# Kernel optimization log

Measured on AMD Instinct MI355X. Metric: run time of the kernel, lower is better.

The kernel has to match this reference:

```python
import jax, jax.numpy as jnp
import numpy as np

BATCH, C_IN, C_OUT, N_GRID, N_MODES = 64, 64, 64, 8192, 64
SCALE = 1.0 / (C_IN * C_OUT)


def setup_inputs() -> dict:
    key = jax.random.key(0)
    k1, k2, k3 = jax.random.split(key, 3)
    lhss = jax.random.normal(k1, (BATCH, C_IN, N_GRID), dtype=jnp.float32)
    # torch.rand on cfloat draws real and imag uniformly in [0,1), then scaled
    w_real = SCALE * jax.random.uniform(k2, (C_IN, C_OUT, N_MODES), dtype=jnp.float32)
    w_imag = SCALE * jax.random.uniform(k3, (C_IN, C_OUT, N_MODES), dtype=jnp.float32)
    return {"lhss": lhss, "w_real": w_real, "w_imag": w_imag}


def reference(lhss, w_real, w_imag):
    n = lhss.shape[-1]
    n_freq = n // 2 + 1  # rfft output length
    weights = w_real + 1j * w_imag  # (c_in, c_out, modes), complex64
    xf = jnp.fft.rfft(lhss)  # (b, c_in, n_freq) complex
    # complex channel-mixing on the first N_MODES frequency bins only
    mixed = jnp.einsum("bix,iox->box", xf[:, :, :N_MODES], weights)
    # zero-pad remaining high-frequency bins, then inverse rfft
    res = jnp.zeros((lhss.shape[0], weights.shape[1], n_freq), dtype=mixed.dtype)
    res = res.at[:, :, :N_MODES].set(mixed)
    return jnp.fft.irfft(res, n=n)
```

## Files before the change

kernel.cpp:

```cpp
#include <hip/hip_runtime.h>
#include <hip/hip_bf16.h>

#define NG 8192
#define NB 64
#define CI 64
#define CO 64
#define NM 64
#define NFJ 128
#define NROWS 4096

typedef __bf16 bf16x8 __attribute__((ext_vector_type(8)));
typedef float f32x4 __attribute__((ext_vector_type(4)));

#define GLOAD_LDS16(gsrc, ldst)                                                   \
    __builtin_amdgcn_global_load_lds(                                             \
        (const __attribute__((address_space(1))) void*)(gsrc),                    \
        (__attribute__((address_space(3))) void*)(ldst), 16, 0, 0)


__global__ __launch_bounds__(256) void sc_prep(const float* __restrict__ wr,
                                               const float* __restrict__ wi,
                                               __bf16* __restrict__ Ft,
                                               __bf16* __restrict__ Ginv,
                                               __bf16* __restrict__ Wtf) {
    __shared__ __align__(16) __bf16 wlds[16384];
    const float W0 = 6.2831853071795864769f / (float)NG;
    if (blockIdx.x >= 64) {
        int idx = (blockIdx.x - 64) * 256 + threadIdx.x;
        if (idx < 128 * NG) {
            int j = idx >> 13, pos = idx & (NG - 1);
            int blk = pos >> 6, g = (pos >> 3) & 7, e = pos & 7;
            int ksrc = (blk << 6) + (((g ^ (j & 7)) << 3) | e);
            int m = j >> 1;
            int t = (m * ksrc) & (NG - 1);
            float s, c;
            __sincosf((float)t * W0, &s, &c);
            Ft[idx] = (__bf16)((j & 1) ? -s : c);
        } else {
            int i2 = idx - 128 * NG;
            int n = i2 >> 7, pos = i2 & 127;
            int g = pos >> 3, e = pos & 7;
            int psrc = ((g ^ (n & 15)) << 3) | e;
            int m = psrc >> 1, im = psrc & 1;
            int t = (m * n) & (NG - 1);
            float s, c;
            __sincosf((float)t * W0, &s, &c);
            float v;
            if (im) v = (m == 0) ? 0.0f : (-2.0f / NG) * s;
            else    v = ((m == 0) ? 1.0f : 2.0f) / NG * c;
            Ginv[i2] = (__bf16)v;
        }
    } else {
        const int m = blockIdx.x;
        const int t = threadIdx.x;
        const int o = t & 63, q = t >> 6;
        const int ot = o >> 4, l = o & 15;
        float wrv[16], wiv[16];
        #pragma unroll
        for (int cc = 0; cc < 16; ++cc) {
            int ci = q * 16 + cc;
            wrv[cc] = wr[((size_t)ci * 64 + o) * 64 + m];
            wiv[cc] = wi[((size_t)ci * 64 + o) * 64 + m];
        }
        #pragma unroll
        for (int cc = 0; cc < 16; ++cc) {
            int ci = q * 16 + cc;
            int ksa = ci >> 5, ksb = 2 + ksa;
            int kg = (ci >> 3) & 3, e = ci & 7;
            int pos = (kg * 16 + l) * 8 + e;
            wlds[(0*16 + ksa*4 + ot)*512 + pos] = (__bf16)wrv[cc];
            wlds[(0*16 + ksb*4 + ot)*512 + pos] = (__bf16)(-wiv[cc]);
            wlds[(1*16 + ksa*4 + ot)*512 + pos] = (__bf16)wiv[cc];
            wlds[(1*16 + ksb*4 + ot)*512 + pos] = (__bf16)wrv[cc];
        }
        __syncthreads();
        const uint4* src = (const uint4*)wlds;
        uint4* dst = (uint4*)(Wtf + (size_t)m * 16384);
        #pragma unroll
        for (int s = 0; s < 8; ++s)
            dst[s * 256 + t] = src[s * 256 + t];
    }
}

__global__ __launch_bounds__(256) void sc_dft(const float* __restrict__ A,
                                              const __bf16* __restrict__ Ft,
                                              float* __restrict__ XFp,
                                              int nsteps) {
    __shared__ __align__(16) char smem[40960];
    char* A0 = smem;
    char* A1 = smem + 4096;
    char* F0 = smem + 8192;
    char* F1 = smem + 24576;

    const int tid = threadIdx.x;
    const int w = tid >> 6, lane = tid & 63;
    const int l15 = lane & 15, kg = lane >> 4;
    const int wm = w >> 1, wn = w & 1;
    const int rt = blockIdx.x & 127, sp = blockIdx.x >> 7;
    const int r0 = rt * 32;
    const size_t kb0 = (size_t)sp * nsteps * 64;
    const int swz = l15 & 7;

    float4 av[2];
    f32x4 acc[4] = {};

    auto issueA = [&](int step) {
        size_t kb = kb0 + (size_t)step * 64;
        #pragma unroll
        for (int s = 0; s < 2; ++s) {
            int c = s * 256 + tid;
            av[s] = *(const float4*)(A + (size_t)(r0 + (c >> 4)) * NG + kb + (c & 15) * 4);
        }
    };
    auto writeA = [&](char* Ab) {
        #pragma unroll
        for (int s = 0; s < 2; ++s) {
            int c = s * 256 + tid, row = c >> 4, cq = c & 15;
            union { __bf16 h[4]; uint2 u; } cv;
            cv.h[0] = (__bf16)av[s].x; cv.h[1] = (__bf16)av[s].y;
            cv.h[2] = (__bf16)av[s].z; cv.h[3] = (__bf16)av[s].w;
            *(uint2*)(Ab + row * 128 + (((cq >> 1) ^ (row & 7)) << 4) + ((cq & 1) << 3)) = cv.u;
        }
    };
    auto stageF = [&](int step, char* Fb) {
        size_t kb = kb0 + (size_t)step * 64;
        #pragma unroll
        for (int s = 0; s < 4; ++s) {
            int cc = s * 256 + tid;
            GLOAD_LDS16(Ft + (size_t)(cc >> 3) * NG + kb + (cc & 7) * 8, Fb + cc * 16);
        }
    };
    auto compute = [&](const char* Ab, const char* Fb) {
        #pragma unroll
        for (int ks2 = 0; ks2 < 2; ++ks2) {
            bf16x8 a, b[4];
            a = *(const bf16x8*)(Ab + (wm*16 + l15) * 128 +
                                 (((ks2*4 + kg) ^ swz) << 4));
            #pragma unroll
            for (int jt = 0; jt < 4; ++jt)
                b[jt] = *(const bf16x8*)(Fb + (wn*64 + jt*16 + l15) * 128 +
                                         (((ks2*4 + kg) ^ swz) << 4));
            #pragma unroll
            for (int jt = 0; jt < 4; ++jt)
                acc[jt] = __builtin_amdgcn_mfma_f32_16x16x32_bf16(
                    a, b[jt], acc[jt], 0, 0, 0);
        }
    };

    issueA(0); stageF(0, F0); writeA(A0);
    __syncthreads();
    for (int t = 0; t < nsteps; ++t) {
        char* Ac = (t & 1) ? A1 : A0;
        char* Fc = (t & 1) ? F1 : F0;
        char* An = (t & 1) ? A0 : A1;
        char* Fn = (t & 1) ? F0 : F1;
        if (t + 1 < nsteps) { issueA(t + 1); stageF(t + 1, Fn); }
        compute(Ac, Fc);
        if (t + 1 < nsteps) writeA(An);
        __syncthreads();
    }
    #pragma unroll
    for (int jt = 0; jt < 4; ++jt)
        *(f32x4*)(XFp + ((size_t)sp * NFJ + wn*64 + jt*16 + l15) * NROWS +
                  (r0 + wm*16 + kg*4)) = acc[jt];
}

__global__ __launch_bounds__(256) void sc_mix(const float* __restrict__ XFp,
                                              const __bf16* __restrict__ Wtf,
                                              __bf16* __restrict__ M2, int nsplit) {
    __shared__ __align__(16) char at[4096];
    const int t = threadIdx.x;
    const int k = blockIdx.x >> 2, bq = blockIdx.x & 3;
    const int lane = t & 63, ot = t >> 6;
    const int l15 = lane & 15, kg = lane >> 4;

    const int c = t >> 7, t127 = t & 127;
    f32x4 s0 = {}, s1 = {};
    {
        const float* src = XFp + (size_t)(2*k + c) * NROWS + bq*1024 + t127*8;
        const size_t pstride = (size_t)NFJ * NROWS;
        if (nsplit == 8) {
            #pragma unroll
            for (int p = 0; p < 8; ++p) {
                s0 += *(const f32x4*)(src + p*pstride);
                s1 += *(const f32x4*)(src + p*pstride + 4);
            }
        } else {
            for (int p = 0; p < nsplit; ++p) {
                s0 += *(const f32x4*)(src + p*pstride);
                s1 += *(const f32x4*)(src + p*pstride + 4);
            }
        }
    }
    {
        const int bl = t127 >> 3;
        const int i0 = (t127 & 7) * 8;
        union { __bf16 h[8]; uint4 u; } cv;
        cv.h[0]=(__bf16)s0[0]; cv.h[1]=(__bf16)s0[1];
        cv.h[2]=(__bf16)s0[2]; cv.h[3]=(__bf16)s0[3];
        cv.h[4]=(__bf16)s1[0]; cv.h[5]=(__bf16)s1[1];
        cv.h[6]=(__bf16)s1[2]; cv.h[7]=(__bf16)s1[3];
        *(uint4*)(at + bl*256 + ((((c*64 + i0) >> 3) ^ bl) << 4)) = cv.u;
    }
    __syncthreads();

    bf16x8 a[4];
    #pragma unroll
    for (int ks = 0; ks < 4; ++ks)
        a[ks] = *(const bf16x8*)(at + l15*256 + (((ks*4 + kg) ^ l15) << 4));

    f32x4 accR = {}, accI = {};
    #pragma unroll
    for (int ks = 0; ks < 4; ++ks) {
        bf16x8 b0 = *(const bf16x8*)(Wtf + (size_t)(((k*2+0)*4+ks)*4+ot)*512 + lane*8);
        accR = __builtin_amdgcn_mfma_f32_16x16x32_bf16(a[ks], b0, accR, 0, 0, 0);
    }
    #pragma unroll
    for (int ks = 0; ks < 4; ++ks) {
        bf16x8 b1 = *(const bf16x8*)(Wtf + (size_t)(((k*2+1)*4+ks)*4+ot)*512 + lane*8);
        accI = __builtin_amdgcn_mfma_f32_16x16x32_bf16(a[ks], b1, accI, 0, 0, 0);
    }
    #pragma unroll
    for (int rr = 0; rr < 4; ++rr) {
        int bg = bq*16 + kg*4 + rr;
        size_t r = (size_t)bg * CO + ot*16 + l15;
        ushort2 pk;
        pk.x = __builtin_bit_cast(unsigned short, (__bf16)accR[rr]);
        pk.y = __builtin_bit_cast(unsigned short, (__bf16)accI[rr]);
        *(ushort2*)(M2 + r * NFJ + 2 * k) = pk;
    }
}

__global__ __launch_bounds__(512) void sc_idft(const __bf16* __restrict__ M2,
                                               const __bf16* __restrict__ Ginv,
                                               float* __restrict__ out) {
    __shared__ __align__(16) char gls[32768];
    const int tid = threadIdx.x;
    const int w = tid >> 6, lane = tid & 63;
    const int l15 = lane & 15, kg = lane >> 4;
    const int wm = w >> 1;
    const int wn = w & 1;
    const int r0 = (blockIdx.x >> 6) * 128;
    const int n0 = (blockIdx.x & 63) * 128;

    #pragma unroll
    for (int s = 0; s < 4; ++s) {
        int cc = s * 512 + tid;
        GLOAD_LDS16(Ginv + (size_t)n0 * NFJ + cc * 8, gls + cc * 16);
    }

    bf16x8 af[2][4];
    #pragma unroll
    for (int mt = 0; mt < 2; ++mt)
        #pragma unroll
        for (int ks = 0; ks < 4; ++ks)
            af[mt][ks] = *(const bf16x8*)(M2 + (size_t)(r0 + wm*32 + mt*16 + l15) * NFJ +
                                          ks*32 + kg*8);
    __syncthreads();

    f32x4 acc[2][4] = {};
    #pragma unroll
    for (int nt = 0; nt < 4; ++nt) {
        int row = wn*64 + nt*16 + l15;
        bf16x8 bfr[4];
        #pragma unroll
        for (int ks = 0; ks < 4; ++ks)
            bfr[ks] = *(const bf16x8*)(gls + row * 256 + (((ks*4 + kg) ^ (row & 15)) << 4));
        #pragma unroll
        for (int mt = 0; mt < 2; ++mt)
            #pragma unroll
            for (int ks = 0; ks < 4; ++ks)
                acc[mt][nt] = __builtin_amdgcn_mfma_f32_16x16x32_bf16(
                    bfr[ks], af[mt][ks], acc[mt][nt], 0, 0, 0);
    }
    #pragma unroll
    for (int mt = 0; mt < 2; ++mt)
        #pragma unroll
        for (int nt = 0; nt < 4; ++nt)
            *(f32x4*)(out + (size_t)(r0 + wm*32 + mt*16 + l15) * NG +
                      n0 + wn*64 + nt*16 + kg*4) = acc[mt][nt];
}

extern "C" void kernel_launch(void* const* d_in, const int* in_sizes, int n_in,
                              void* d_out, int out_size, void* d_ws, size_t ws_size,
                              hipStream_t stream) {
    const float* lhss = (const float*)d_in[0];
    const float* w_real = (const float*)d_in[1];
    const float* w_imag = (const float*)d_in[2];
    float* out = (float*)d_out;

    char* ws = (char*)d_ws;
    __bf16* Ft_sw   = (__bf16*)ws;
    __bf16* Ginv_sw = (__bf16*)(ws + (2u << 20));
    __bf16* M2      = (__bf16*)(ws + (6u << 20));
    __bf16* Wtf     = (__bf16*)(ws + (7u << 20));
    float*  XFp     = (float*) (ws + (9u << 20));

    int split;
    if      (ws_size >= (25u << 20)) split = 8;
    else if (ws_size >= (17u << 20)) split = 4;
    else if (ws_size >= (13u << 20)) split = 2;
    else                             split = 1;
    int nsteps = 128 / split;

    sc_prep<<<8256, 256, 0, stream>>>(w_real, w_imag, Ft_sw, Ginv_sw, Wtf);
    sc_dft<<<128 * split, 256, 0, stream>>>(lhss, Ft_sw, XFp, nsteps);
    sc_mix<<<256, 256, 0, stream>>>(XFp, Wtf, M2, split);
    sc_idft<<<2048, 512, 0, stream>>>(M2, Ginv_sw, out);
}
```

Before: 105.8 us.

## Double DFT block row tile and stage F through registers instead of LDS-direct loads

```diff
diff --git a/kernel.cpp b/kernel.cpp
--- a/kernel.cpp
+++ b/kernel.cpp
@@ -86,83 +86,100 @@
                                               const __bf16* __restrict__ Ft,
                                               float* __restrict__ XFp,
                                               int nsteps) {
-    __shared__ __align__(16) char smem[40960];
-    char* A0 = smem;
-    char* A1 = smem + 4096;
-    char* F0 = smem + 8192;
-    char* F1 = smem + 24576;
+    __shared__ __align__(16) char smem[49152];
+    char* Ab0 = smem;
+    char* Ab1 = smem + 8192;
+    char* Fb0 = smem + 16384;
+    char* Fb1 = smem + 32768;
 
     const int tid = threadIdx.x;
     const int w = tid >> 6, lane = tid & 63;
     const int l15 = lane & 15, kg = lane >> 4;
     const int wm = w >> 1, wn = w & 1;
-    const int rt = blockIdx.x & 127, sp = blockIdx.x >> 7;
-    const int r0 = rt * 32;
+    const int rt = blockIdx.x & 63, sp = blockIdx.x >> 6;
+    const int r0 = rt * 64;
     const size_t kb0 = (size_t)sp * nsteps * 64;
     const int swz = l15 & 7;
 
-    float4 av[2];
-    f32x4 acc[4] = {};
-
-    auto issueA = [&](int step) {
+    float4 av0[4], av1[4];
+    uint4  fv0[4], fv1[4];
+    f32x4 acc[2][4] = {};
+
+    auto loadA = [&](int step, float4 (&av)[4]) {
         size_t kb = kb0 + (size_t)step * 64;
         #pragma unroll
-        for (int s = 0; s < 2; ++s) {
+        for (int s = 0; s < 4; ++s) {
             int c = s * 256 + tid;
             av[s] = *(const float4*)(A + (size_t)(r0 + (c >> 4)) * NG + kb + (c & 15) * 4);
         }
     };
-    auto writeA = [&](char* Ab) {
-        #pragma unroll
-        for (int s = 0; s < 2; ++s) {
+    auto loadF = [&](int step, uint4 (&fv)[4]) {
+        size_t kb = kb0 + (size_t)step * 64;
+        #pragma unroll
+        for (int s = 0; s < 4; ++s) {
+            int cc = s * 256 + tid;
+            fv[s] = *(const uint4*)(Ft + (size_t)(cc >> 3) * NG + kb + (cc & 7) * 8);
+        }
+    };
+    auto writeT = [&](const float4 (&av)[4], const uint4 (&fv)[4],
+                      char* Ad, char* Fd) {
+        #pragma unroll
+        for (int s = 0; s < 4; ++s) {
             int c = s * 256 + tid, row = c >> 4, cq = c & 15;
             union { __bf16 h[4]; uint2 u; } cv;
             cv.h[0] = (__bf16)av[s].x; cv.h[1] = (__bf16)av[s].y;
             cv.h[2] = (__bf16)av[s].z; cv.h[3] = (__bf16)av[s].w;
-            *(uint2*)(Ab + row * 128 + (((cq >> 1) ^ (row & 7)) << 4) + ((cq & 1) << 3)) = cv.u;
-        }
-    };
-    auto stageF = [&](int step, char* Fb) {
-        size_t kb = kb0 + (size_t)step * 64;
+            *(uint2*)(Ad + row * 128 + (((cq >> 1) ^ (row & 7)) << 4) + ((cq & 1) << 3)) = cv.u;
+        }
         #pragma unroll
         for (int s = 0; s < 4; ++s) {
             int cc = s * 256 + tid;
-            GLOAD_LDS16(Ft + (size_t)(cc >> 3) * NG + kb + (cc & 7) * 8, Fb + cc * 16);
+            *(uint4*)(Fd + cc * 16) = fv[s];
         }
     };
     auto compute = [&](const char* Ab, const char* Fb) {
         #pragma unroll
         for (int ks2 = 0; ks2 < 2; ++ks2) {
-            bf16x8 a, b[4];
-            a = *(const bf16x8*)(Ab + (wm*16 + l15) * 128 +
-                                 (((ks2*4 + kg) ^ swz) << 4));
+            bf16x8 a[2], b[4];
+            #pragma unroll
+            for (int mt = 0; mt < 2; ++mt)
+                a[mt] = *(const bf16x8*)(Ab + (wm*32 + mt*16 + l15) * 128 +
+                                         (((ks2*4 + kg) ^ swz) << 4));
             #pragma unroll
             for (int jt = 0; jt < 4; ++jt)
                 b[jt] = *(const bf16x8*)(Fb + (wn*64 + jt*16 + l15) * 128 +
                                          (((ks2*4 + kg) ^ swz) << 4));
             #pragma unroll
-            for (int jt = 0; jt < 4; ++jt)
-                acc[jt] = __builtin_amdgcn_mfma_f32_16x16x32_bf16(
-                    a, b[jt], acc[jt], 0, 0, 0);
+            for (int mt = 0; mt < 2; ++mt)
+                #pragma unroll
+                for (int jt = 0; jt < 4; ++jt)
+                    acc[mt][jt] = __builtin_amdgcn_mfma_f32_16x16x32_bf16(
+                        a[mt], b[jt], acc[mt][jt], 0, 0, 0);
         }
     };
 
-    issueA(0); stageF(0, F0); writeA(A0);
+    loadA(0, av0); loadF(0, fv0);
+    writeT(av0, fv0, Ab0, Fb0);
+    loadA(1, av1); loadF(1, fv1);
     __syncthreads();
-    for (int t = 0; t < nsteps; ++t) {
-        char* Ac = (t & 1) ? A1 : A0;
-        char* Fc = (t & 1) ? F1 : F0;
-        char* An = (t & 1) ? A0 : A1;
-        char* Fn = (t & 1) ? F0 : F1;
-        if (t + 1 < nsteps) { issueA(t + 1); stageF(t + 1, Fn); }
-        compute(Ac, Fc);
-        if (t + 1 < nsteps) writeA(An);
+
+    for (int t = 0; t < nsteps; t += 2) {
+        if (t + 2 < nsteps) { loadA(t + 2, av0); loadF(t + 2, fv0); }
+        compute(Ab0, Fb0);
+        writeT(av1, fv1, Ab1, Fb1);
         __syncthreads();
-    }
-    #pragma unroll
-    for (int jt = 0; jt < 4; ++jt)
-        *(f32x4*)(XFp + ((size_t)sp * NFJ + wn*64 + jt*16 + l15) * NROWS +
-                  (r0 + wm*16 + kg*4)) = acc[jt];
+        if (t + 3 < nsteps) { loadA(t + 3, av1); loadF(t + 3, fv1); }
+        compute(Ab1, Fb1);
+        if (t + 2 < nsteps) writeT(av0, fv0, Ab0, Fb0);
+        __syncthreads();
+    }
+
+    #pragma unroll
+    for (int mt = 0; mt < 2; ++mt)
+        #pragma unroll
+        for (int jt = 0; jt < 4; ++jt)
+            *(f32x4*)(XFp + ((size_t)sp * NFJ + wn*64 + jt*16 + l15) * NROWS +
+                      (r0 + wm*32 + mt*16 + kg*4)) = acc[mt][jt];
 }
 
 __global__ __launch_bounds__(256) void sc_mix(const float* __restrict__ XFp,
@@ -304,7 +321,7 @@
     int nsteps = 128 / split;
 
     sc_prep<<<8256, 256, 0, stream>>>(w_real, w_imag, Ft_sw, Ginv_sw, Wtf);
-    sc_dft<<<128 * split, 256, 0, stream>>>(lhss, Ft_sw, XFp, nsteps);
+    sc_dft<<<64 * split, 256, 0, stream>>>(lhss, Ft_sw, XFp, nsteps);
     sc_mix<<<256, 256, 0, stream>>>(XFp, Wtf, M2, split);
     sc_idft<<<2048, 512, 0, stream>>>(M2, Ginv_sw, out);
 }
```

Measured after the change: 146.5 us. 1.38x slower.

## Store DFT twiddles in MFMA fragment layout and load them straight into registers

Applied to the files above, without the earlier changes.

```diff
diff --git a/kernel.cpp b/kernel.cpp
--- a/kernel.cpp
+++ b/kernel.cpp
@@ -20,7 +20,7 @@
 
 __global__ __launch_bounds__(256) void sc_prep(const float* __restrict__ wr,
                                                const float* __restrict__ wi,
-                                               __bf16* __restrict__ Ft,
+                                               __bf16* __restrict__ Ftf,
                                                __bf16* __restrict__ Ginv,
                                                __bf16* __restrict__ Wtf) {
     __shared__ __align__(16) __bf16 wlds[16384];
@@ -28,14 +28,16 @@
     if (blockIdx.x >= 64) {
         int idx = (blockIdx.x - 64) * 256 + threadIdx.x;
         if (idx < 128 * NG) {
-            int j = idx >> 13, pos = idx & (NG - 1);
-            int blk = pos >> 6, g = (pos >> 3) & 7, e = pos & 7;
-            int ksrc = (blk << 6) + (((g ^ (j & 7)) << 3) | e);
+            int e = idx & 7, ln = (idx >> 3) & 63, j16 = (idx >> 9) & 7;
+            int kk = idx >> 12;
+            int kg_ = ln >> 4, l15_ = ln & 15;
+            int j = j16 * 16 + l15_;
+            int k = kk * 32 + kg_ * 8 + e;
             int m = j >> 1;
-            int t = (m * ksrc) & (NG - 1);
+            int t = (m * k) & (NG - 1);
             float s, c;
             __sincosf((float)t * W0, &s, &c);
-            Ft[idx] = (__bf16)((j & 1) ? -s : c);
+            Ftf[idx] = (__bf16)((j & 1) ? -s : c);
         } else {
             int i2 = idx - 128 * NG;
             int n = i2 >> 7, pos = i2 & 127;
@@ -82,15 +84,13 @@
     }
 }
 
-__global__ __launch_bounds__(256) void sc_dft(const float* __restrict__ A,
-                                              const __bf16* __restrict__ Ft,
-                                              float* __restrict__ XFp,
-                                              int nsteps) {
-    __shared__ __align__(16) char smem[40960];
-    char* A0 = smem;
-    char* A1 = smem + 4096;
-    char* F0 = smem + 8192;
-    char* F1 = smem + 24576;
+__global__ __launch_bounds__(256, 4) void sc_dft(const float* __restrict__ A,
+                                                 const __bf16* __restrict__ Ftf,
+                                                 float* __restrict__ XFp,
+                                                 int nsteps) {
+    __shared__ __align__(16) char smem[8192];
+    char* Ab0 = smem;
+    char* Ab1 = smem + 4096;
 
     const int tid = threadIdx.x;
     const int w = tid >> 6, lane = tid & 63;
@@ -100,11 +100,17 @@
     const int r0 = rt * 32;
     const size_t kb0 = (size_t)sp * nsteps * 64;
     const int swz = l15 & 7;
-
-    float4 av[2];
+    const int arow = (wm * 16 + l15) * 128;
+
+    const __bf16* fp = Ftf + (size_t)(wn * 4) * 512 + (size_t)lane * 8;
+    const size_t kkbase = (kb0 >> 5) * 4096;
+
+    float4 avA[2], avB[2];
+    uint4 F0_0, F0_1, F0_2, F0_3, F0_4, F0_5, F0_6, F0_7;
+    uint4 F1_0, F1_1, F1_2, F1_3, F1_4, F1_5, F1_6, F1_7;
     f32x4 acc[4] = {};
 
-    auto issueA = [&](int step) {
+    auto issueA = [&](int step, float4 (&av)[2]) {
         size_t kb = kb0 + (size_t)step * 64;
         #pragma unroll
         for (int s = 0; s < 2; ++s) {
@@ -112,7 +118,7 @@
             av[s] = *(const float4*)(A + (size_t)(r0 + (c >> 4)) * NG + kb + (c & 15) * 4);
         }
     };
-    auto writeA = [&](char* Ab) {
+    auto writeA = [&](const float4 (&av)[2], char* Ab) {
         #pragma unroll
         for (int s = 0; s < 2; ++s) {
             int c = s * 256 + tid, row = c >> 4, cq = c & 15;
@@ -122,43 +128,74 @@
             *(uint2*)(Ab + row * 128 + (((cq >> 1) ^ (row & 7)) << 4) + ((cq & 1) << 3)) = cv.u;
         }
     };
-    auto stageF = [&](int step, char* Fb) {
-        size_t kb = kb0 + (size_t)step * 64;
-        #pragma unroll
-        for (int s = 0; s < 4; ++s) {
-            int cc = s * 256 + tid;
-            GLOAD_LDS16(Ft + (size_t)(cc >> 3) * NG + kb + (cc & 7) * 8, Fb + cc * 16);
-        }
-    };
-    auto compute = [&](const char* Ab, const char* Fb) {
-        #pragma unroll
-        for (int ks2 = 0; ks2 < 2; ++ks2) {
-            bf16x8 a, b[4];
-            a = *(const bf16x8*)(Ab + (wm*16 + l15) * 128 +
-                                 (((ks2*4 + kg) ^ swz) << 4));
-            #pragma unroll
-            for (int jt = 0; jt < 4; ++jt)
-                b[jt] = *(const bf16x8*)(Fb + (wn*64 + jt*16 + l15) * 128 +
-                                         (((ks2*4 + kg) ^ swz) << 4));
-            #pragma unroll
-            for (int jt = 0; jt < 4; ++jt)
-                acc[jt] = __builtin_amdgcn_mfma_f32_16x16x32_bf16(
-                    a, b[jt], acc[jt], 0, 0, 0);
-        }
-    };
-
-    issueA(0); stageF(0, F0); writeA(A0);
-    __syncthreads();
-    for (int t = 0; t < nsteps; ++t) {
-        char* Ac = (t & 1) ? A1 : A0;
-        char* Fc = (t & 1) ? F1 : F0;
-        char* An = (t & 1) ? A0 : A1;
-        char* Fn = (t & 1) ? F0 : F1;
-        if (t + 1 < nsteps) { issueA(t + 1); stageF(t + 1, Fn); }
-        compute(Ac, Fc);
-        if (t + 1 < nsteps) writeA(An);
-        __syncthreads();
-    }
+
+#define MFMA_ __builtin_amdgcn_mfma_f32_16x16x32_bf16
+#define BC_(x) __builtin_bit_cast(bf16x8, x)
+#define LOADF(S, t_)                                                          \
+    {                                                                         \
+        const __bf16* fb_ = fp + kkbase + (size_t)(t_) * 8192;                \
+        F##S##_0 = *(const uint4*)(fb_);                                      \
+        F##S##_1 = *(const uint4*)(fb_ + 512);                                \
+        F##S##_2 = *(const uint4*)(fb_ + 1024);                               \
+        F##S##_3 = *(const uint4*)(fb_ + 1536);                               \
+        F##S##_4 = *(const uint4*)(fb_ + 4096);                               \
+        F##S##_5 = *(const uint4*)(fb_ + 4608);                               \
+        F##S##_6 = *(const uint4*)(fb_ + 5120);                               \
+        F##S##_7 = *(const uint4*)(fb_ + 5632);                               \
+    }
+#define COMP(S, Ab)                                                           \
+    {                                                                         \
+        bf16x8 a0 = *(const bf16x8*)((Ab) + arow + (((0 + kg) ^ swz) << 4));  \
+        acc[0] = MFMA_(a0, BC_(F##S##_0), acc[0], 0, 0, 0);                   \
+        acc[1] = MFMA_(a0, BC_(F##S##_1), acc[1], 0, 0, 0);                   \
+        acc[2] = MFMA_(a0, BC_(F##S##_2), acc[2], 0, 0, 0);                   \
+        acc[3] = MFMA_(a0, BC_(F##S##_3), acc[3], 0, 0, 0);                   \
+        bf16x8 a1 = *(const bf16x8*)((Ab) + arow + (((4 + kg) ^ swz) << 4));  \
+        acc[0] = MFMA_(a1, BC_(F##S##_4), acc[0], 0, 0, 0);                   \
+        acc[1] = MFMA_(a1, BC_(F##S##_5), acc[1], 0, 0, 0);                   \
+        acc[2] = MFMA_(a1, BC_(F##S##_6), acc[2], 0, 0, 0);                   \
+        acc[3] = MFMA_(a1, BC_(F##S##_7), acc[3], 0, 0, 0);                   \
+    }
+#define SB __builtin_amdgcn_sched_barrier(0)
+
+    issueA(0, avA); SB;
+    LOADF(0, 0) SB;
+    writeA(avA, Ab0);
+    issueA(1, avB); SB;
+    asm volatile("s_waitcnt vmcnt(2)" ::: "memory");
+    asm volatile("s_waitcnt lgkmcnt(0)" ::: "memory");
+    __builtin_amdgcn_s_barrier(); SB;
+
+    for (int t = 0; t < nsteps; t += 2) {
+        const bool lp = (t + 2 >= nsteps);
+        LOADF(1, t + 1) SB;
+        if (!lp) issueA(t + 2, avA);
+        SB;
+        COMP(0, Ab0)
+        writeA(avB, Ab1);
+        if (lp) asm volatile("s_waitcnt vmcnt(0)" ::: "memory");
+        else    asm volatile("s_waitcnt vmcnt(2)" ::: "memory");
+        asm volatile("s_waitcnt lgkmcnt(0)" ::: "memory");
+        __builtin_amdgcn_s_barrier(); SB;
+        if (!lp) {
+            LOADF(0, t + 2) SB;
+            issueA(t + 3, avB);
+            SB;
+            COMP(1, Ab1)
+            writeA(avA, Ab0);
+            asm volatile("s_waitcnt vmcnt(2)" ::: "memory");
+            asm volatile("s_waitcnt lgkmcnt(0)" ::: "memory");
+            __builtin_amdgcn_s_barrier(); SB;
+        } else {
+            COMP(1, Ab1)
+        }
+    }
+#undef LOADF
+#undef COMP
+#undef MFMA_
+#undef BC_
+#undef SB
+
     #pragma unroll
     for (int jt = 0; jt < 4; ++jt)
         *(f32x4*)(XFp + ((size_t)sp * NFJ + wn*64 + jt*16 + l15) * NROWS +
@@ -290,7 +327,7 @@
     float* out = (float*)d_out;
 
     char* ws = (char*)d_ws;
-    __bf16* Ft_sw   = (__bf16*)ws;
+    __bf16* Ftf     = (__bf16*)ws;
     __bf16* Ginv_sw = (__bf16*)(ws + (2u << 20));
     __bf16* M2      = (__bf16*)(ws + (6u << 20));
     __bf16* Wtf     = (__bf16*)(ws + (7u << 20));
@@ -303,8 +340,8 @@
     else                             split = 1;
     int nsteps = 128 / split;
 
-    sc_prep<<<8256, 256, 0, stream>>>(w_real, w_imag, Ft_sw, Ginv_sw, Wtf);
-    sc_dft<<<128 * split, 256, 0, stream>>>(lhss, Ft_sw, XFp, nsteps);
+    sc_prep<<<8256, 256, 0, stream>>>(w_real, w_imag, Ftf, Ginv_sw, Wtf);
+    sc_dft<<<128 * split, 256, 0, stream>>>(lhss, Ftf, XFp, nsteps);
     sc_mix<<<256, 256, 0, stream>>>(XFp, Wtf, M2, split);
     sc_idft<<<2048, 512, 0, stream>>>(M2, Ginv_sw, out);
 }
```

After: 128.2 us. +21.2%, slower.
